# Kernel optimization log

Measured on AMD Instinct MI355X. Metric: run time of the kernel, lower is better.

## Reference

```python
import jax, jax.numpy as jnp
import numpy as np

WINDOW_SIZE = 64  # matches init_kwargs


def _local_allowed_mask(L, window_size):
    # Original torch code: for query i, keys in slice [max(i-w//2,0) : min(i+w//2, L)) are allowed.
    half = window_size // 2
    i = jnp.arange(L)[:, None]
    j = jnp.arange(L)[None, :]
    return (j >= i - half) & (j < i + half)  # [L, L] bool, True = attend


def setup_inputs() -> dict:
    key = jax.random.key(0)
    kq, kk, kv = jax.random.split(key, 3)
    B, L, H, E, D = 4, 2048, 16, 64, 64
    queries = jax.random.normal(kq, (B, L, H, E), dtype=jnp.float32)
    keys = jax.random.normal(kk, (B, L, H, E), dtype=jnp.float32)
    values = jax.random.normal(kv, (B, L, H, D), dtype=jnp.float32)
    attn_mask = jnp.zeros((1,), dtype=bool)  # unused by the module
    return {"queries": queries, "keys": keys, "values": values, "attn_mask": attn_mask}


def reference(queries, keys, values, attn_mask):
    B, L, H, E = queries.shape
    scale = 1.0 / np.sqrt(E).astype(np.float32)
    allowed = _local_allowed_mask(L, WINDOW_SIZE)  # [L, L]
    # Dense scores, as in the original module (einsum 'blhe,bshe->bhls')
    scores = jnp.einsum('blhe,bshe->bhls', queries, keys)
    neg_inf = jnp.asarray(-jnp.inf, dtype=scores.dtype)
    scores = jnp.where(allowed[None, None, :, :], scores, neg_inf)
    A = jax.nn.softmax(scale * scores, axis=-1)  # [B, H, L, S]
    V = jnp.einsum('bhls,bshd->blhd', A, values)  # [B, L, H, D]
    return V
```

## Files before the change

kernel.cpp:

```cpp
#include <hip/hip_runtime.h>


#define B_ 4
#define L_ 2048
#define H_ 16
#define E_ 64
#define D_ 64
#define VT_STRIDE 152

typedef __attribute__((ext_vector_type(8))) short short8;
typedef __attribute__((ext_vector_type(4))) float f32x4;

__device__ __forceinline__ unsigned int f2bf(float x) {
  unsigned int b = __float_as_uint(x);
  b += 0x7fffu + ((b >> 16) & 1u);
  return b >> 16;
}
__device__ __forceinline__ unsigned int pack2(float a, float b) {
  return f2bf(a) | (f2bf(b) << 16);
}
__device__ __forceinline__ short8 pack8(const f32x4& a, const f32x4& b) {
  union { short8 s; uint4 u; } r;
  r.u = make_uint4(pack2(a[0], a[1]), pack2(a[2], a[3]),
                   pack2(b[0], b[1]), pack2(b[2], b[3]));
  return r.s;
}
__device__ __forceinline__ int clampL(int k) {
  return k < 0 ? 0 : (k > (L_ - 1) ? (L_ - 1) : k);
}

__global__ __launch_bounds__(256, 8)
void local_attn_mfma(const float* __restrict__ qg,
                     const float* __restrict__ kg,
                     const float* __restrict__ vg,
                     float* __restrict__ og) {
  __shared__ __align__(16) unsigned short Vt[64 * VT_STRIDE];

  const int t = threadIdx.x;
  const int q0 = blockIdx.x * 64;
  const int h = blockIdx.y;
  const int b = blockIdx.z;
  const int kstart = q0 - 32;
  const int wave = t >> 6;
  const int lane = t & 63;
  const int col16 = lane & 15;
  const int quad = lane >> 4;

  const int kp = t >> 2;
  const int dq = t & 3;
  f32x4 va[4], vc[4];
  {
    const int k0 = clampL(kstart + 2 * kp);
    const int k1 = clampL(kstart + 2 * kp + 1);
    const float* p0 = vg + ((size_t)(b * L_ + k0) * H_ + h) * D_ + dq * 16;
    const float* p1 = vg + ((size_t)(b * L_ + k1) * H_ + h) * D_ + dq * 16;
    #pragma unroll
    for (int i = 0; i < 4; ++i) va[i] = *(const f32x4*)(p0 + i * 4);
    #pragma unroll
    for (int i = 0; i < 4; ++i) vc[i] = *(const f32x4*)(p1 + i * 4);
  }

  short8 qa0, qa1;
  {
    const float* pq = qg + ((size_t)(b * L_ + q0 + wave * 16 + col16) * H_ + h) * E_ + quad * 8;
    f32x4 qf0 = *(const f32x4*)pq;
    f32x4 qf1 = *(const f32x4*)(pq + 4);
    f32x4 qf2 = *(const f32x4*)(pq + 32);
    f32x4 qf3 = *(const f32x4*)(pq + 36);
    qa0 = pack8(qf0, qf1);
    qa1 = pack8(qf2, qf3);
  }

  #pragma unroll
  for (int i = 0; i < 4; ++i)
    #pragma unroll
    for (int j = 0; j < 4; ++j) {
      int d = dq * 16 + i * 4 + j;
      *(unsigned int*)&Vt[d * VT_STRIDE + 2 * kp] = pack2(va[i][j], vc[i][j]);
    }
  *(uint2*)&Vt[(t >> 2) * VT_STRIDE + 128 + (t & 3) * 4] = make_uint2(0u, 0u);

  __syncthreads();

  f32x4 acc[5];
  #pragma unroll
  for (int tt = 0; tt < 5; ++tt) {
    const int key = clampL(kstart + wave * 16 + tt * 16 + col16);
    const float* pk = kg + ((size_t)(b * L_ + key) * H_ + h) * E_ + quad * 8;
    f32x4 k0 = *(const f32x4*)pk;
    f32x4 k1 = *(const f32x4*)(pk + 4);
    f32x4 k2 = *(const f32x4*)(pk + 32);
    f32x4 k3 = *(const f32x4*)(pk + 36);
    short8 kb0 = pack8(k0, k1);
    short8 kb1 = pack8(k2, k3);
    f32x4 c = {0.f, 0.f, 0.f, 0.f};
    c = __builtin_amdgcn_mfma_f32_16x16x32_bf16(kb0, qa0, c, 0, 0, 0);
    c = __builtin_amdgcn_mfma_f32_16x16x32_bf16(kb1, qa1, c, 0, 0, 0);
    acc[tt] = c;
  }

  float mx = -1e30f;
  #pragma unroll
  for (int tt = 0; tt < 5; ++tt)
    #pragma unroll
    for (int r = 0; r < 4; ++r) {
      const int k_loc = tt * 16 + quad * 4 + r;
      const int gkey = kstart + wave * 16 + k_loc;
      const bool ok = (k_loc >= col16) && (k_loc < col16 + 64) &&
                      (gkey >= 0) && (gkey < L_);
      const float v = ok ? acc[tt][r] * 0.125f : -1e30f;
      acc[tt][r] = v;
      mx = fmaxf(mx, v);
    }
  mx = fmaxf(mx, __shfl_xor(mx, 16));
  mx = fmaxf(mx, __shfl_xor(mx, 32));
  float s = 0.f;
  #pragma unroll
  for (int tt = 0; tt < 5; ++tt)
    #pragma unroll
    for (int r = 0; r < 4; ++r) {
      const float e = __expf(acc[tt][r] - mx);
      acc[tt][r] = e;
      s += e;
    }
  s += __shfl_xor(s, 16);
  s += __shfl_xor(s, 32);
  const float inv = 1.0f / s;

  short8 pa[3];
  {
    union { short8 s8; uint4 u4; } w;
    w.u4 = make_uint4(pack2(acc[0][0] * inv, acc[0][1] * inv),
                      pack2(acc[0][2] * inv, acc[0][3] * inv),
                      pack2(acc[1][0] * inv, acc[1][1] * inv),
                      pack2(acc[1][2] * inv, acc[1][3] * inv));
    pa[0] = w.s8;
    w.u4 = make_uint4(pack2(acc[2][0] * inv, acc[2][1] * inv),
                      pack2(acc[2][2] * inv, acc[2][3] * inv),
                      pack2(acc[3][0] * inv, acc[3][1] * inv),
                      pack2(acc[3][2] * inv, acc[3][3] * inv));
    pa[1] = w.s8;
    w.u4 = make_uint4(pack2(acc[4][0] * inv, acc[4][1] * inv),
                      pack2(acc[4][2] * inv, acc[4][3] * inv), 0u, 0u);
    pa[2] = w.s8;
  }

  f32x4 oacc[4];
  #pragma unroll
  for (int nt = 0; nt < 4; ++nt) oacc[nt] = (f32x4){0.f, 0.f, 0.f, 0.f};
  #pragma unroll
  for (int nt = 0; nt < 4; ++nt) {
    const int rowb = (nt * 16 + col16) * VT_STRIDE;
    #pragma unroll
    for (int ks = 0; ks < 3; ++ks) {
      union { short8 s8; uint2 u2[2]; } vb;
      vb.u2[0] = *(const uint2*)&Vt[rowb + wave * 16 + ks * 32 + quad * 4];
      vb.u2[1] = *(const uint2*)&Vt[rowb + wave * 16 + ks * 32 + 16 + quad * 4];
      oacc[nt] = __builtin_amdgcn_mfma_f32_16x16x32_bf16(pa[ks], vb.s8, oacc[nt], 0, 0, 0);
    }
  }

  #pragma unroll
  for (int r = 0; r < 4; ++r) {
    const int q = q0 + wave * 16 + quad * 4 + r;
    float* orow = og + ((size_t)(b * L_ + q) * H_ + h) * D_;
    #pragma unroll
    for (int nt = 0; nt < 4; ++nt)
      orow[nt * 16 + col16] = oacc[nt][r];
  }
}

extern "C" void kernel_launch(void* const* d_in, const int* in_sizes, int n_in,
                              void* d_out, int out_size, void* d_ws, size_t ws_size,
                              hipStream_t stream) {
  const float* q = (const float*)d_in[0];
  const float* k = (const float*)d_in[1];
  const float* v = (const float*)d_in[2];
  float* o = (float*)d_out;
  dim3 grid(L_ / 64, H_, B_);
  local_attn_mfma<<<grid, dim3(256), 0, stream>>>(q, k, v, o);
}
```

Baseline: 152.6 us.

## Stage shared key tile in LDS via async global-to-LDS loads

The block's 128-row key tile is now loaded once into a 32 KB fp32 shared buffer with an XOR swizzle, using global_load_lds direct-to-LDS transfers. Before, each wave re-read its overlapping key rows from global memory. The Q bf16 packing is also moved after the V transpose so it overlaps the loads. This cuts redundant global and L2 traffic on keys. In exchange, LDS use grows and the occupancy hint drops from 8 to 3 blocks, which lowers latency hiding.

```diff
diff --git a/kernel.cpp b/kernel.cpp
--- a/kernel.cpp
+++ b/kernel.cpp
@@ -29,11 +29,12 @@
   return k < 0 ? 0 : (k > (L_ - 1) ? (L_ - 1) : k);
 }
 
-__global__ __launch_bounds__(256, 8)
+__global__ __launch_bounds__(256, 3)
 void local_attn_mfma(const float* __restrict__ qg,
                      const float* __restrict__ kg,
                      const float* __restrict__ vg,
                      float* __restrict__ og) {
+  __shared__ __align__(16) float Ks32[128 * 64];
   __shared__ __align__(16) unsigned short Vt[64 * VT_STRIDE];
 
   const int t = threadIdx.x;
@@ -59,16 +60,26 @@
     #pragma unroll
     for (int i = 0; i < 4; ++i) vc[i] = *(const f32x4*)(p1 + i * 4);
   }
-
-  short8 qa0, qa1;
+  f32x4 qf0, qf1, qf2, qf3;
   {
     const float* pq = qg + ((size_t)(b * L_ + q0 + wave * 16 + col16) * H_ + h) * E_ + quad * 8;
-    f32x4 qf0 = *(const f32x4*)pq;
-    f32x4 qf1 = *(const f32x4*)(pq + 4);
-    f32x4 qf2 = *(const f32x4*)(pq + 32);
-    f32x4 qf3 = *(const f32x4*)(pq + 36);
-    qa0 = pack8(qf0, qf1);
-    qa1 = pack8(qf2, qf3);
+    qf0 = *(const f32x4*)pq;
+    qf1 = *(const f32x4*)(pq + 4);
+    qf2 = *(const f32x4*)(pq + 32);
+    qf3 = *(const f32x4*)(pq + 36);
+  }
+
+  #pragma unroll
+  for (int it = 0; it < 8; ++it) {
+    const int cid = t + it * 256;
+    const int row = cid >> 4, ch = cid & 15;
+    const int chs = ch ^ (row & 15);
+    const int key = clampL(kstart + row);
+    const float* src = kg + ((size_t)(b * L_ + key) * H_ + h) * E_ + chs * 4;
+    float* dst = &Ks32[(it * 256 + wave * 64) * 4];
+    __builtin_amdgcn_global_load_lds(
+        (__attribute__((address_space(1))) void*)src,
+        (__attribute__((address_space(3))) void*)dst, 16, 0, 0);
   }
 
   #pragma unroll
@@ -80,17 +91,24 @@
     }
   *(uint2*)&Vt[(t >> 2) * VT_STRIDE + 128 + (t & 3) * 4] = make_uint2(0u, 0u);
 
+  const short8 qa0 = pack8(qf0, qf1);
+  const short8 qa1 = pack8(qf2, qf3);
+
   __syncthreads();
 
+  const int c0 = (2 * quad) ^ col16;
+  const int c1 = (2 * quad + 1) ^ col16;
+  const int c2 = (2 * quad + 8) ^ col16;
+  const int c3 = (2 * quad + 9) ^ col16;
   f32x4 acc[5];
   #pragma unroll
   for (int tt = 0; tt < 5; ++tt) {
-    const int key = clampL(kstart + wave * 16 + tt * 16 + col16);
-    const float* pk = kg + ((size_t)(b * L_ + key) * H_ + h) * E_ + quad * 8;
-    f32x4 k0 = *(const f32x4*)pk;
-    f32x4 k1 = *(const f32x4*)(pk + 4);
-    f32x4 k2 = *(const f32x4*)(pk + 32);
-    f32x4 k3 = *(const f32x4*)(pk + 36);
+    const int krow = wave * 16 + tt * 16 + col16;
+    const float* Kr = &Ks32[krow * 64];
+    f32x4 k0 = *(const f32x4*)(Kr + c0 * 4);
+    f32x4 k1 = *(const f32x4*)(Kr + c1 * 4);
+    f32x4 k2 = *(const f32x4*)(Kr + c2 * 4);
+    f32x4 k3 = *(const f32x4*)(Kr + c3 * 4);
     short8 kb0 = pack8(k0, k1);
     short8 kb1 = pack8(k2, k3);
     f32x4 c = {0.f, 0.f, 0.f, 0.f};
```

Result: faster. 136.7 us (-10.4%).

## Switch to single-wave blocks of 16 queries with per-wave V staging

Applied to the files above, without the earlier changes.

Each block becomes a single 64-lane wave handling 16 queries instead of four waves handling 64. Each wave stages its own 80-key V window into LDS, so the cross-wave dependency on shared V is gone. The K tile loads are hoisted ahead of the MFMAs. This buys more independent blocks and less synchronisation stall, at the cost of reloading overlapping V and K windows (80 keys per 16 queries versus 128 per 64), which raises global memory traffic.

```diff
diff --git a/kernel.cpp b/kernel.cpp
--- a/kernel.cpp
+++ b/kernel.cpp
@@ -6,7 +6,7 @@
 #define H_ 16
 #define E_ 64
 #define D_ 64
-#define VT_STRIDE 152
+#define VSTR 104
 
 typedef __attribute__((ext_vector_type(8))) short short8;
 typedef __attribute__((ext_vector_type(4))) float f32x4;
@@ -29,73 +29,65 @@
   return k < 0 ? 0 : (k > (L_ - 1) ? (L_ - 1) : k);
 }
 
-__global__ __launch_bounds__(256, 8)
+__global__ __launch_bounds__(64, 3)
 void local_attn_mfma(const float* __restrict__ qg,
                      const float* __restrict__ kg,
                      const float* __restrict__ vg,
                      float* __restrict__ og) {
-  __shared__ __align__(16) unsigned short Vt[64 * VT_STRIDE];
+  __shared__ __align__(16) unsigned short Vt[64 * VSTR];
 
-  const int t = threadIdx.x;
-  const int q0 = blockIdx.x * 64;
+  const int lane = threadIdx.x;
+  const int q0 = blockIdx.x * 16;
   const int h = blockIdx.y;
   const int b = blockIdx.z;
   const int kstart = q0 - 32;
-  const int wave = t >> 6;
-  const int lane = t & 63;
   const int col16 = lane & 15;
   const int quad = lane >> 4;
 
-  const int kp = t >> 2;
-  const int dq = t & 3;
-  f32x4 va[4], vc[4];
-  {
-    const int k0 = clampL(kstart + 2 * kp);
-    const int k1 = clampL(kstart + 2 * kp + 1);
-    const float* p0 = vg + ((size_t)(b * L_ + k0) * H_ + h) * D_ + dq * 16;
-    const float* p1 = vg + ((size_t)(b * L_ + k1) * H_ + h) * D_ + dq * 16;
+  const int p2 = (lane >> 3) * 2;
+  const int o8 = (lane & 7) * 8;
+  #pragma unroll
+  for (int c = 0; c < 5; ++c) {
+    const int k0 = clampL(kstart + c * 16 + p2);
+    const int k1 = clampL(kstart + c * 16 + p2 + 1);
+    const float* pv0 = vg + ((size_t)(b * L_ + k0) * H_ + h) * D_ + o8;
+    const float* pv1 = vg + ((size_t)(b * L_ + k1) * H_ + h) * D_ + o8;
+    const f32x4 a0 = *(const f32x4*)pv0;
+    const f32x4 a1 = *(const f32x4*)(pv0 + 4);
+    const f32x4 b0 = *(const f32x4*)pv1;
+    const f32x4 b1 = *(const f32x4*)(pv1 + 4);
     #pragma unroll
-    for (int i = 0; i < 4; ++i) va[i] = *(const f32x4*)(p0 + i * 4);
-    #pragma unroll
-    for (int i = 0; i < 4; ++i) vc[i] = *(const f32x4*)(p1 + i * 4);
+    for (int j = 0; j < 4; ++j) {
+      *(unsigned int*)&Vt[(o8 + j) * VSTR + c * 16 + p2] = pack2(a0[j], b0[j]);
+      *(unsigned int*)&Vt[(o8 + 4 + j) * VSTR + c * 16 + p2] = pack2(a1[j], b1[j]);
+    }
   }
+  #pragma unroll
+  for (int i = 0; i < 4; ++i)
+    *(uint2*)&Vt[lane * VSTR + 80 + i * 4] = make_uint2(0u, 0u);
 
   short8 qa0, qa1;
   {
-    const float* pq = qg + ((size_t)(b * L_ + q0 + wave * 16 + col16) * H_ + h) * E_ + quad * 8;
-    f32x4 qf0 = *(const f32x4*)pq;
-    f32x4 qf1 = *(const f32x4*)(pq + 4);
-    f32x4 qf2 = *(const f32x4*)(pq + 32);
-    f32x4 qf3 = *(const f32x4*)(pq + 36);
-    qa0 = pack8(qf0, qf1);
-    qa1 = pack8(qf2, qf3);
+    const float* pq = qg + ((size_t)(b * L_ + q0 + col16) * H_ + h) * E_ + quad * 8;
+    qa0 = pack8(*(const f32x4*)pq, *(const f32x4*)(pq + 4));
+    qa1 = pack8(*(const f32x4*)(pq + 32), *(const f32x4*)(pq + 36));
   }
 
+  short8 kb0[5], kb1[5];
   #pragma unroll
-  for (int i = 0; i < 4; ++i)
-    #pragma unroll
-    for (int j = 0; j < 4; ++j) {
-      int d = dq * 16 + i * 4 + j;
-      *(unsigned int*)&Vt[d * VT_STRIDE + 2 * kp] = pack2(va[i][j], vc[i][j]);
-    }
-  *(uint2*)&Vt[(t >> 2) * VT_STRIDE + 128 + (t & 3) * 4] = make_uint2(0u, 0u);
-
-  __syncthreads();
+  for (int tt = 0; tt < 5; ++tt) {
+    const int key = clampL(kstart + tt * 16 + col16);
+    const float* pk = kg + ((size_t)(b * L_ + key) * H_ + h) * E_ + quad * 8;
+    kb0[tt] = pack8(*(const f32x4*)pk, *(const f32x4*)(pk + 4));
+    kb1[tt] = pack8(*(const f32x4*)(pk + 32), *(const f32x4*)(pk + 36));
+  }
 
   f32x4 acc[5];
   #pragma unroll
   for (int tt = 0; tt < 5; ++tt) {
-    const int key = clampL(kstart + wave * 16 + tt * 16 + col16);
-    const float* pk = kg + ((size_t)(b * L_ + key) * H_ + h) * E_ + quad * 8;
-    f32x4 k0 = *(const f32x4*)pk;
-    f32x4 k1 = *(const f32x4*)(pk + 4);
-    f32x4 k2 = *(const f32x4*)(pk + 32);
-    f32x4 k3 = *(const f32x4*)(pk + 36);
-    short8 kb0 = pack8(k0, k1);
-    short8 kb1 = pack8(k2, k3);
     f32x4 c = {0.f, 0.f, 0.f, 0.f};
-    c = __builtin_amdgcn_mfma_f32_16x16x32_bf16(kb0, qa0, c, 0, 0, 0);
-    c = __builtin_amdgcn_mfma_f32_16x16x32_bf16(kb1, qa1, c, 0, 0, 0);
+    c = __builtin_amdgcn_mfma_f32_16x16x32_bf16(kb0[tt], qa0, c, 0, 0, 0);
+    c = __builtin_amdgcn_mfma_f32_16x16x32_bf16(kb1[tt], qa1, c, 0, 0, 0);
     acc[tt] = c;
   }
 
@@ -105,9 +97,9 @@
     #pragma unroll
     for (int r = 0; r < 4; ++r) {
       const int k_loc = tt * 16 + quad * 4 + r;
-      const int gkey = kstart + wave * 16 + k_loc;
-      const bool ok = (k_loc >= col16) && (k_loc < col16 + 64) &&
-                      (gkey >= 0) && (gkey < L_);
+      const int gkey = kstart + k_loc;
+      const bool ok = ((unsigned)(k_loc - col16) < 64u) &&
+                      ((unsigned)gkey < (unsigned)L_);
       const float v = ok ? acc[tt][r] * 0.125f : -1e30f;
       acc[tt][r] = v;
       mx = fmaxf(mx, v);
@@ -145,24 +137,26 @@
     pa[2] = w.s8;
   }
 
+  __syncthreads();
+
   f32x4 oacc[4];
   #pragma unroll
   for (int nt = 0; nt < 4; ++nt) oacc[nt] = (f32x4){0.f, 0.f, 0.f, 0.f};
   #pragma unroll
   for (int nt = 0; nt < 4; ++nt) {
-    const int rowb = (nt * 16 + col16) * VT_STRIDE;
+    const int rowb = (nt * 16 + col16) * VSTR;
     #pragma unroll
     for (int ks = 0; ks < 3; ++ks) {
       union { short8 s8; uint2 u2[2]; } vb;
-      vb.u2[0] = *(const uint2*)&Vt[rowb + wave * 16 + ks * 32 + quad * 4];
-      vb.u2[1] = *(const uint2*)&Vt[rowb + wave * 16 + ks * 32 + 16 + quad * 4];
+      vb.u2[0] = *(const uint2*)&Vt[rowb + ks * 32 + quad * 4];
+      vb.u2[1] = *(const uint2*)&Vt[rowb + ks * 32 + 16 + quad * 4];
       oacc[nt] = __builtin_amdgcn_mfma_f32_16x16x32_bf16(pa[ks], vb.s8, oacc[nt], 0, 0, 0);
     }
   }
 
   #pragma unroll
   for (int r = 0; r < 4; ++r) {
-    const int q = q0 + wave * 16 + quad * 4 + r;
+    const int q = q0 + quad * 4 + r;
     float* orow = og + ((size_t)(b * L_ + q) * H_ + h) * D_;
     #pragma unroll
     for (int nt = 0; nt < 4; ++nt)
@@ -177,6 +171,6 @@
   const float* k = (const float*)d_in[1];
   const float* v = (const float*)d_in[2];
   float* o = (float*)d_out;
-  dim3 grid(L_ / 64, H_, B_);
-  local_attn_mfma<<<grid, dim3(256), 0, stream>>>(q, k, v, o);
+  dim3 grid(L_ / 16, H_, B_);
+  local_attn_mfma<<<grid, dim3(64), 0, stream>>>(q, k, v, o);
 }
```

Result: slower. 169.4 us (+11.0%).
